# Kernel optimization log

Hardware: AMD Instinct MI355X
Metric: run time of the kernel (lower is better)

Reference implementation:

```python
import jax, jax.numpy as jnp
import numpy as np

# init config (matches init_kwargs)
NO_TRANS = False
SPATIAL_SCALE = 0.0625
POOLED = 7
SAMPLES = 2          # sampling_ratio (sample_per_part)
TRANS_STD = 0.1

B, C, H, W = 2, 256, 96, 96
N_ROIS = 512


def setup_inputs() -> dict:
    key = jax.random.key(0)
    k1, k2, k3, k4, k5 = jax.random.split(key, 5)
    bottom_data = jax.random.normal(k1, (B, C, H, W), dtype=jnp.float32)
    img = H / SPATIAL_SCALE  # image-space extent (1536)
    bidx = jax.random.randint(k2, (N_ROIS,), 0, B).astype(jnp.float32)
    xy1 = jax.random.uniform(k3, (N_ROIS, 2), minval=0.0, maxval=0.7 * img)
    wh = jax.random.uniform(k4, (N_ROIS, 2), minval=0.05 * img, maxval=0.3 * img)
    bottom_rois = jnp.concatenate([bidx[:, None], xy1, xy1 + wh], axis=1)  # [N,5]
    bottom_trans = jax.random.normal(k5, (N_ROIS, 2, POOLED, POOLED), dtype=jnp.float32)
    return {"bottom_data": bottom_data, "bottom_rois": bottom_rois, "bottom_trans": bottom_trans}


def _deform_psroi_pool(feat, rois, trans):
    # feat [B,C,H,W], rois [N,5], trans [N,2,P,P] -> out [N,C,P,P]
    Hf, Wf = feat.shape[2], feat.shape[3]
    b = rois[:, 0].astype(jnp.int32)                                    # [N]
    # CUDA kernel rounds roi coords, shifts by -0.5
    x1 = jnp.round(rois[:, 1]) * SPATIAL_SCALE - 0.5
    y1 = jnp.round(rois[:, 2]) * SPATIAL_SCALE - 0.5
    x2 = (jnp.round(rois[:, 3]) + 1.0) * SPATIAL_SCALE - 0.5
    y2 = (jnp.round(rois[:, 4]) + 1.0) * SPATIAL_SCALE - 0.5
    rw = jnp.maximum(x2 - x1, 0.1)
    rh = jnp.maximum(y2 - y1, 0.1)
    bin_w = rw / POOLED
    bin_h = rh / POOLED
    sub_w = bin_w / SAMPLES
    sub_h = bin_h / SAMPLES

    grid = jnp.arange(POOLED, dtype=feat.dtype)
    # part_size == pooled_size and group_size == 1 -> part_h=ph, part_w=pw, class 0
    if NO_TRANS:
        trans_x = jnp.zeros((rois.shape[0], POOLED, POOLED), feat.dtype)
        trans_y = trans_x
    else:
        trans_x = trans[:, 0] * TRANS_STD  # [N,P,P]
        trans_y = trans[:, 1] * TRANS_STD

    # bin start coords per (n, ph, pw)
    wstart = grid[None, None, :] * bin_w[:, None, None] + x1[:, None, None] + trans_x * rw[:, None, None]
    hstart = grid[None, :, None] * bin_h[:, None, None] + y1[:, None, None] + trans_y * rh[:, None, None]

    s = jnp.arange(SAMPLES, dtype=feat.dtype)
    # sample coords [N,P,P,S(ih),S(iw)]
    w = wstart[:, :, :, None, None] + s[None, None, None, None, :] * sub_w[:, None, None, None, None]
    h = hstart[:, :, :, None, None] + s[None, None, None, :, None] * sub_h[:, None, None, None, None]

    valid = (w >= -0.5) & (w <= Wf - 0.5) & (h >= -0.5) & (h <= Hf - 0.5)
    wc = jnp.clip(w, 0.0, Wf - 1.0)
    hc = jnp.clip(h, 0.0, Hf - 1.0)
    x0 = jnp.floor(wc); y0 = jnp.floor(hc)
    dx = wc - x0; dy = hc - y0
    x0i = x0.astype(jnp.int32); y0i = y0.astype(jnp.int32)
    x1i = jnp.ceil(wc).astype(jnp.int32); y1i = jnp.ceil(hc).astype(jnp.int32)

    feat_hwc = jnp.transpose(feat, (0, 2, 3, 1))  # [B,H,W,C]
    bb = b[:, None, None, None, None]

    def gather(yi, xi):
        return feat_hwc[bb, yi, xi]  # [N,P,P,S,S,C]

    w00 = ((1.0 - dx) * (1.0 - dy))[..., None]
    w01 = (dx * (1.0 - dy))[..., None]
    w10 = ((1.0 - dx) * dy)[..., None]
    w11 = (dx * dy)[..., None]
    val = (w00 * gather(y0i, x0i) + w01 * gather(y0i, x1i)
           + w10 * gather(y1i, x0i) + w11 * gather(y1i, x1i))
    val = jnp.where(valid[..., None], val, 0.0)

    ssum = val.sum(axis=(3, 4))                              # [N,P,P,C]
    count = valid.astype(feat.dtype).sum(axis=(3, 4))        # [N,P,P]
    out = jnp.where(count[..., None] > 0, ssum / jnp.maximum(count[..., None], 1.0), 0.0)
    return jnp.transpose(out, (0, 3, 1, 2))                  # [N,C,P,P]


def reference(bottom_data, bottom_rois, bottom_trans):
    return _deform_psroi_pool(bottom_data, bottom_rois, bottom_trans)
```

## Files before the change

### kernel.cpp

```cpp
#include <hip/hip_runtime.h>

#define B_      2
#define C_      256
#define H_      96
#define W_      96
#define P_      7
#define NROIS_  512
#define SCALE_  0.0625f
#define TSTD_   0.1f

__global__ __launch_bounds__(256) void nchw_to_nhwc(const float* __restrict__ in,
                                                    float* __restrict__ out) {
    __shared__ float tile[32][33];
    const int b  = blockIdx.z;
    const int p0 = blockIdx.x * 32;
    const int c0 = blockIdx.y * 32;
    const int tx = threadIdx.x;
    const int ty = threadIdx.y;
    const float* src = in  + (size_t)b * (C_ * H_ * W_);
    float*       dst = out + (size_t)b * (C_ * H_ * W_);
#pragma unroll
    for (int k = 0; k < 32; k += 8)
        tile[ty + k][tx] = src[(size_t)(c0 + ty + k) * (H_ * W_) + p0 + tx];
    __syncthreads();
#pragma unroll
    for (int k = 0; k < 32; k += 8)
        dst[(size_t)(p0 + ty + k) * C_ + c0 + tx] = tile[tx][ty + k];
}

template <bool HWC>
__global__ __launch_bounds__(256) void dpsroi_pool(const float* __restrict__ feat,
                                                   const float* __restrict__ rois,
                                                   const float* __restrict__ trans,
                                                   float* __restrict__ out) {
    __shared__ float sout[C_ * P_ * P_];

    const int n    = blockIdx.x;
    const int tid  = threadIdx.x;
    const int wave = tid >> 6;
    const int lane = tid & 63;

    const float r0  = rois[n * 5 + 0];
    const float rx1 = rois[n * 5 + 1];
    const float ry1 = rois[n * 5 + 2];
    const float rx2 = rois[n * 5 + 3];
    const float ry2 = rois[n * 5 + 4];
    const int   broi = (int)r0;
    const float x1 = rintf(rx1) * SCALE_ - 0.5f;
    const float y1 = rintf(ry1) * SCALE_ - 0.5f;
    const float x2 = (rintf(rx2) + 1.0f) * SCALE_ - 0.5f;
    const float y2 = (rintf(ry2) + 1.0f) * SCALE_ - 0.5f;
    const float rw = fmaxf(x2 - x1, 0.1f);
    const float rh = fmaxf(y2 - y1, 0.1f);
    const float bin_w = rw / 7.0f;
    const float bin_h = rh / 7.0f;
    const float sub_w = bin_w * 0.5f;
    const float sub_h = bin_h * 0.5f;

    for (int bin = wave; bin < P_ * P_; bin += 4) {
        const int pi = bin / P_;
        const int pj = bin % P_;

        const float tx = trans[((n * 2 + 0) * P_ + pi) * P_ + pj] * TSTD_;
        const float ty = trans[((n * 2 + 1) * P_ + pi) * P_ + pj] * TSTD_;
        const float wstart = (float)pj * bin_w + x1 + tx * rw;
        const float hstart = (float)pi * bin_h + y1 + ty * rh;

        float acc0 = 0.f, acc1 = 0.f, acc2 = 0.f, acc3 = 0.f;
        int cnt = 0;
#pragma unroll
        for (int sa = 0; sa < 2; ++sa) {
#pragma unroll
            for (int sb = 0; sb < 2; ++sb) {
                const float w = wstart + (float)sb * sub_w;
                const float h = hstart + (float)sa * sub_h;
                if (w >= -0.5f && w <= (float)W_ - 0.5f &&
                    h >= -0.5f && h <= (float)H_ - 0.5f) {
                    ++cnt;
                    const float wc  = fminf(fmaxf(w, 0.0f), (float)(W_ - 1));
                    const float hc  = fminf(fmaxf(h, 0.0f), (float)(H_ - 1));
                    const float x0f = floorf(wc), y0f = floorf(hc);
                    const float dx  = wc - x0f,   dy  = hc - y0f;
                    const int   x0  = (int)x0f,   y0  = (int)y0f;
                    const int   xp  = (int)ceilf(wc), yp = (int)ceilf(hc);
                    const float w00 = (1.0f - dx) * (1.0f - dy);
                    const float w01 = dx * (1.0f - dy);
                    const float w10 = (1.0f - dx) * dy;
                    const float w11 = dx * dy;

                    if (HWC) {
                        const float* fb = feat + (size_t)broi * (H_ * W_ * C_);
                        const float4* p00 = (const float4*)(fb + ((size_t)y0 * W_ + x0) * C_) + lane;
                        const float4* p01 = (const float4*)(fb + ((size_t)y0 * W_ + xp) * C_) + lane;
                        const float4* p10 = (const float4*)(fb + ((size_t)yp * W_ + x0) * C_) + lane;
                        const float4* p11 = (const float4*)(fb + ((size_t)yp * W_ + xp) * C_) + lane;
                        const float4 v00 = *p00;
                        const float4 v01 = *p01;
                        const float4 v10 = *p10;
                        const float4 v11 = *p11;
                        acc0 += w00 * v00.x + w01 * v01.x + w10 * v10.x + w11 * v11.x;
                        acc1 += w00 * v00.y + w01 * v01.y + w10 * v10.y + w11 * v11.y;
                        acc2 += w00 * v00.z + w01 * v01.z + w10 * v10.z + w11 * v11.z;
                        acc3 += w00 * v00.w + w01 * v01.w + w10 * v10.w + w11 * v11.w;
                    } else {
                        float a[4];
#pragma unroll
                        for (int k = 0; k < 4; ++k) {
                            const int c = 4 * lane + k;
                            const float* fc = feat + (((size_t)broi * C_ + c) * H_) * W_;
                            const float v00 = fc[(size_t)y0 * W_ + x0];
                            const float v01 = fc[(size_t)y0 * W_ + xp];
                            const float v10 = fc[(size_t)yp * W_ + x0];
                            const float v11 = fc[(size_t)yp * W_ + xp];
                            a[k] = w00 * v00 + w01 * v01 + w10 * v10 + w11 * v11;
                        }
                        acc0 += a[0]; acc1 += a[1]; acc2 += a[2]; acc3 += a[3];
                    }
                }
            }
        }

        const float inv = (cnt > 0) ? (1.0f / (float)cnt) : 0.0f;
        const int c4 = 4 * lane;
        sout[(c4 + 0) * (P_ * P_) + bin] = acc0 * inv;
        sout[(c4 + 1) * (P_ * P_) + bin] = acc1 * inv;
        sout[(c4 + 2) * (P_ * P_) + bin] = acc2 * inv;
        sout[(c4 + 3) * (P_ * P_) + bin] = acc3 * inv;
    }

    __syncthreads();
    float* outn = out + (size_t)n * (C_ * P_ * P_);
    for (int f = tid; f < C_ * P_ * P_; f += 256)
        outn[f] = sout[f];
}

extern "C" void kernel_launch(void* const* d_in, const int* in_sizes, int n_in,
                              void* d_out, int out_size, void* d_ws, size_t ws_size,
                              hipStream_t stream) {
    const float* feat  = (const float*)d_in[0];
    const float* rois  = (const float*)d_in[1];
    const float* trans = (const float*)d_in[2];
    float* out = (float*)d_out;

    const size_t need = (size_t)B_ * C_ * H_ * W_ * sizeof(float);
    if (ws_size >= need) {
        float* hwc = (float*)d_ws;
        dim3 tb(32, 8);
        dim3 tg((H_ * W_) / 32, C_ / 32, B_);
        nchw_to_nhwc<<<tg, tb, 0, stream>>>(feat, hwc);
        dpsroi_pool<true><<<NROIS_, 256, 0, stream>>>(hwc, rois, trans, out);
    } else {
        dpsroi_pool<false><<<NROIS_, 256, 0, stream>>>(feat, rois, trans, out);
    }
}
```

Measured before the change: 109.6 us.

## Split channels across 8 blocks per ROI for more parallelism in pooling

The pooling kernel now launches 8 blocks per ROI, each handling 32 channels. Within a block, 8 threads cover the channels with float4 loads and 32 bins run in parallel, where before each wave handled one bin across all 256 channels. This raises the block count from 512 to 4096 and shrinks shared memory per block, which should improve occupancy and latency hiding on the gather loads. The NCHW fallback path is removed, so the code now always uses the workspace transpose without checking the workspace size.

```diff
diff --git a/kernel.cpp b/kernel.cpp
--- a/kernel.cpp
+++ b/kernel.cpp
@@ -8,6 +8,9 @@
 #define NROIS_  512
 #define SCALE_  0.0625f
 #define TSTD_   0.1f
+
+#define NGROUP_ 8
+#define GC_     (C_ / NGROUP_)
 
 __global__ __launch_bounds__(256) void nchw_to_nhwc(const float* __restrict__ in,
                                                     float* __restrict__ out) {
@@ -28,38 +31,36 @@
         dst[(size_t)(p0 + ty + k) * C_ + c0 + tx] = tile[tx][ty + k];
 }
 
-template <bool HWC>
-__global__ __launch_bounds__(256) void dpsroi_pool(const float* __restrict__ feat,
-                                                   const float* __restrict__ rois,
-                                                   const float* __restrict__ trans,
-                                                   float* __restrict__ out) {
-    __shared__ float sout[C_ * P_ * P_];
+__global__ __launch_bounds__(256) void dpsroi_pool2(const float* __restrict__ feat,
+                                                    const float* __restrict__ rois,
+                                                    const float* __restrict__ trans,
+                                                    float* __restrict__ out) {
+    __shared__ float sout[GC_ * P_ * P_];
 
-    const int n    = blockIdx.x;
-    const int tid  = threadIdx.x;
-    const int wave = tid >> 6;
-    const int lane = tid & 63;
+    const int blk = blockIdx.x;
+    const int g   = blk & (NGROUP_ - 1);
+    const int n   = blk >> 3;
+    const int tid = threadIdx.x;
+    const int cl  = (tid & 7) * 4;
+    const int cab = g * GC_ + cl;
 
-    const float r0  = rois[n * 5 + 0];
-    const float rx1 = rois[n * 5 + 1];
-    const float ry1 = rois[n * 5 + 2];
-    const float rx2 = rois[n * 5 + 3];
-    const float ry2 = rois[n * 5 + 4];
-    const int   broi = (int)r0;
-    const float x1 = rintf(rx1) * SCALE_ - 0.5f;
-    const float y1 = rintf(ry1) * SCALE_ - 0.5f;
-    const float x2 = (rintf(rx2) + 1.0f) * SCALE_ - 0.5f;
-    const float y2 = (rintf(ry2) + 1.0f) * SCALE_ - 0.5f;
+    const int   broi = (int)rois[n * 5 + 0];
+    const float x1 = rintf(rois[n * 5 + 1]) * SCALE_ - 0.5f;
+    const float y1 = rintf(rois[n * 5 + 2]) * SCALE_ - 0.5f;
+    const float x2 = (rintf(rois[n * 5 + 3]) + 1.0f) * SCALE_ - 0.5f;
+    const float y2 = (rintf(rois[n * 5 + 4]) + 1.0f) * SCALE_ - 0.5f;
     const float rw = fmaxf(x2 - x1, 0.1f);
     const float rh = fmaxf(y2 - y1, 0.1f);
-    const float bin_w = rw / 7.0f;
-    const float bin_h = rh / 7.0f;
+    const float bin_w = rw * (1.0f / 7.0f);
+    const float bin_h = rh * (1.0f / 7.0f);
     const float sub_w = bin_w * 0.5f;
     const float sub_h = bin_h * 0.5f;
 
-    for (int bin = wave; bin < P_ * P_; bin += 4) {
+    const float* fb = feat + (size_t)broi * (H_ * W_ * C_) + cab;
+
+    for (int bin = tid >> 3; bin < P_ * P_; bin += 32) {
         const int pi = bin / P_;
-        const int pj = bin % P_;
+        const int pj = bin - pi * P_;
 
         const float tx = trans[((n * 2 + 0) * P_ + pi) * P_ + pj] * TSTD_;
         const float ty = trans[((n * 2 + 1) * P_ + pi) * P_ + pj] * TSTD_;
@@ -88,49 +89,28 @@
                     const float w10 = (1.0f - dx) * dy;
                     const float w11 = dx * dy;
 
-                    if (HWC) {
-                        const float* fb = feat + (size_t)broi * (H_ * W_ * C_);
-                        const float4* p00 = (const float4*)(fb + ((size_t)y0 * W_ + x0) * C_) + lane;
-                        const float4* p01 = (const float4*)(fb + ((size_t)y0 * W_ + xp) * C_) + lane;
-                        const float4* p10 = (const float4*)(fb + ((size_t)yp * W_ + x0) * C_) + lane;
-                        const float4* p11 = (const float4*)(fb + ((size_t)yp * W_ + xp) * C_) + lane;
-                        const float4 v00 = *p00;
-                        const float4 v01 = *p01;
-                        const float4 v10 = *p10;
-                        const float4 v11 = *p11;
-                        acc0 += w00 * v00.x + w01 * v01.x + w10 * v10.x + w11 * v11.x;
-                        acc1 += w00 * v00.y + w01 * v01.y + w10 * v10.y + w11 * v11.y;
-                        acc2 += w00 * v00.z + w01 * v01.z + w10 * v10.z + w11 * v11.z;
-                        acc3 += w00 * v00.w + w01 * v01.w + w10 * v10.w + w11 * v11.w;
-                    } else {
-                        float a[4];
-#pragma unroll
-                        for (int k = 0; k < 4; ++k) {
-                            const int c = 4 * lane + k;
-                            const float* fc = feat + (((size_t)broi * C_ + c) * H_) * W_;
-                            const float v00 = fc[(size_t)y0 * W_ + x0];
-                            const float v01 = fc[(size_t)y0 * W_ + xp];
-                            const float v10 = fc[(size_t)yp * W_ + x0];
-                            const float v11 = fc[(size_t)yp * W_ + xp];
-                            a[k] = w00 * v00 + w01 * v01 + w10 * v10 + w11 * v11;
-                        }
-                        acc0 += a[0]; acc1 += a[1]; acc2 += a[2]; acc3 += a[3];
-                    }
+                    const float4 v00 = *(const float4*)(fb + ((size_t)y0 * W_ + x0) * C_);
+                    const float4 v01 = *(const float4*)(fb + ((size_t)y0 * W_ + xp) * C_);
+                    const float4 v10 = *(const float4*)(fb + ((size_t)yp * W_ + x0) * C_);
+                    const float4 v11 = *(const float4*)(fb + ((size_t)yp * W_ + xp) * C_);
+                    acc0 += w00 * v00.x + w01 * v01.x + w10 * v10.x + w11 * v11.x;
+                    acc1 += w00 * v00.y + w01 * v01.y + w10 * v10.y + w11 * v11.y;
+                    acc2 += w00 * v00.z + w01 * v01.z + w10 * v10.z + w11 * v11.z;
+                    acc3 += w00 * v00.w + w01 * v01.w + w10 * v10.w + w11 * v11.w;
                 }
             }
         }
 
         const float inv = (cnt > 0) ? (1.0f / (float)cnt) : 0.0f;
-        const int c4 = 4 * lane;
-        sout[(c4 + 0) * (P_ * P_) + bin] = acc0 * inv;
-        sout[(c4 + 1) * (P_ * P_) + bin] = acc1 * inv;
-        sout[(c4 + 2) * (P_ * P_) + bin] = acc2 * inv;
-        sout[(c4 + 3) * (P_ * P_) + bin] = acc3 * inv;
+        sout[(cl + 0) * (P_ * P_) + bin] = acc0 * inv;
+        sout[(cl + 1) * (P_ * P_) + bin] = acc1 * inv;
+        sout[(cl + 2) * (P_ * P_) + bin] = acc2 * inv;
+        sout[(cl + 3) * (P_ * P_) + bin] = acc3 * inv;
     }
 
     __syncthreads();
-    float* outn = out + (size_t)n * (C_ * P_ * P_);
-    for (int f = tid; f < C_ * P_ * P_; f += 256)
+    float* outn = out + ((size_t)n * C_ + g * GC_) * (P_ * P_);
+    for (int f = tid; f < GC_ * P_ * P_; f += 256)
         outn[f] = sout[f];
 }
 
@@ -142,14 +122,9 @@
     const float* trans = (const float*)d_in[2];
     float* out = (float*)d_out;
 
-    const size_t need = (size_t)B_ * C_ * H_ * W_ * sizeof(float);
-    if (ws_size >= need) {
-        float* hwc = (float*)d_ws;
-        dim3 tb(32, 8);
-        dim3 tg((H_ * W_) / 32, C_ / 32, B_);
-        nchw_to_nhwc<<<tg, tb, 0, stream>>>(feat, hwc);
-        dpsroi_pool<true><<<NROIS_, 256, 0, stream>>>(hwc, rois, trans, out);
-    } else {
-        dpsroi_pool<false><<<NROIS_, 256, 0, stream>>>(feat, rois, trans, out);
-    }
+    float* hwc = (float*)d_ws;
+    dim3 tb(32, 8);
+    dim3 tg((H_ * W_) / 32, C_ / 32, B_);
+    nchw_to_nhwc<<<tg, tb, 0, stream>>>(feat, hwc);
+    dpsroi_pool2<<<NROIS_ * NGROUP_, 256, 0, stream>>>(hwc, rois, trans, out);
 }
```

New measurement: 98.16 us. -10.4%, faster.
